# Kernel optimization log

Measured on AMD Instinct MI355X. Metric: run time of the kernel, lower is better.

The kernel has to match this reference:

```python
import jax, jax.numpy as jnp
import numpy as np

N, E, IN, H, C, ED = 50000, 400000, 128, 16, 32, 16
NEG_SLOPE = 0.2

def setup_inputs() -> dict:
    key = jax.random.key(0)
    ks = jax.random.split(key, 9)
    x = jax.random.normal(ks[0], (N, IN), jnp.float32)
    edge_index = jax.random.randint(ks[1], (2, E), 0, N, dtype=jnp.int32)
    edge_attr = jax.random.normal(ks[2], (E, ED), jnp.float32)
    batch = jnp.zeros((N,), jnp.int32)
    W_l = jax.random.normal(ks[3], (IN, H * C), jnp.float32) * 0.05
    W_r = jax.random.normal(ks[4], (IN, H * C), jnp.float32) * 0.05
    att = jax.random.normal(ks[5], (H, C), jnp.float32) * 0.05
    bias_gat = jax.random.normal(ks[6], (C,), jnp.float32) * 0.05
    W_res = jax.random.normal(ks[7], (IN, C), jnp.float32) * 0.05
    return {"x": x, "edge_index": edge_index, "edge_attr": edge_attr, "batch": batch,
            "W_l": W_l, "W_r": W_r, "att": att, "bias_gat": bias_gat, "W_res": W_res}

def reference(x, edge_index, edge_attr, batch, W_l, W_r, att, bias_gat, W_res):
    # GATv2Conv (heads=16, concat=False, add_self_loops=True, edge_dim=None so
    # edge_attr is unused; dropout is inference no-op), then ReLU + projected residual.
    n = x.shape[0]
    loops = jnp.arange(n, dtype=edge_index.dtype)
    src = jnp.concatenate([edge_index[0], loops])  # message source j
    dst = jnp.concatenate([edge_index[1], loops])  # message target i
    xl = (x @ W_l).reshape(n, H, C)  # source transform
    xr = (x @ W_r).reshape(n, H, C)  # target transform
    # GATv2 score: e_ij = a^T LeakyReLU(xl_j + xr_i), per head. [Etot, H]
    e = jnp.einsum('ehc,hc->eh', jax.nn.leaky_relu(xl[src] + xr[dst], NEG_SLOPE), att)
    # segment softmax over incoming edges of each destination node
    m = jax.lax.stop_gradient(jax.ops.segment_max(e, dst, num_segments=n))
    ex = jnp.exp(e - m[dst])
    s = jax.ops.segment_sum(ex, dst, num_segments=n)
    alpha = ex / (s[dst] + 1e-16)  # [Etot, H]
    # weighted scatter-aggregate of source messages
    out = jax.ops.segment_sum(xl[src] * alpha[:, :, None], dst, num_segments=n)  # [N, H, C]
    gat_out = out.mean(axis=1) + bias_gat  # concat=False -> head mean, + bias
    x_out = jax.nn.relu(gat_out) + x @ W_res  # ReLU then SkipConnection projection
    return (x_out, alpha)
```

## Files before the change

### kernel.cpp

```cpp
#include <hip/hip_runtime.h>
#include <hip/hip_bf16.h>

typedef unsigned int u32;
typedef unsigned short u16;

typedef __attribute__((ext_vector_type(8))) short bf16x8;
typedef __attribute__((ext_vector_type(4))) float f32x4;
typedef __attribute__((ext_vector_type(2))) float f32x2;

__device__ __forceinline__ float bflo(u32 p){ union{u32 u; float f;} v; v.u = p << 16; return v.f; }
__device__ __forceinline__ float bfhi(u32 p){ union{u32 u; float f;} v; v.u = p & 0xFFFF0000u; return v.f; }
__device__ __forceinline__ u16 f2bf(float f){
    union{float f; u32 u;} v; v.f = f;
    u32 r = (v.u + 0x7FFFu + ((v.u >> 16) & 1u)) >> 16;
    return (u16)r;
}
__device__ __forceinline__ u32 pack2(float a, float b){
    return ((u32)f2bf(a)) | (((u32)f2bf(b)) << 16);
}

#define HH 16
#define CC 32
#define HC 512
#define KIN 128
#define CT 1056
#define RESCALE_THR 8.0f

__global__ __launch_bounds__(256) void k_prep(
    const float* __restrict__ x, const float* __restrict__ Wl,
    const float* __restrict__ Wr, const float* __restrict__ Wres,
    u16* __restrict__ xb, u16* __restrict__ wbt_frag, int* __restrict__ counts,
    int xq, int N)
{
    int t = blockIdx.x * 256 + threadIdx.x;
    if (t < xq) {
        const float4* src = (const float4*)(x + (size_t)t * 8);
        float4 a = src[0], b = src[1];
        uint4 o;
        o.x = pack2(a.x, a.y); o.y = pack2(a.z, a.w);
        o.z = pack2(b.x, b.y); o.w = pack2(b.z, b.w);
        ((uint4*)xb)[t] = o;
    } else if (t < xq + CT * 128) {
        int u = t - xq;
        int c = u >> 7;
        int k = u & 127;
        float v;
        if (c < 512)       v = Wl[(size_t)k * 512 + c];
        else if (c < 1024) v = Wr[(size_t)k * 512 + (c - 512)];
        else               v = Wres[(size_t)k * 32 + (c - 1024)];
        int e    = k & 7;
        int krow = k >> 3;
        int kk   = krow >> 2;
        int lane = ((krow & 3) << 4) | (c & 15);
        int ct   = c >> 4;
        wbt_frag[(((size_t)ct * 4 + kk) * 64 + lane) * 8 + e] = f2bf(v);
    } else if (t < xq + CT * 128 + N) {
        counts[t - xq - CT * 128] = 0;
    }
}

__global__ __launch_bounds__(256) void k_mfma(
    const u16* __restrict__ xb, const u16* __restrict__ wbt_frag,
    u16* __restrict__ xl, u16* __restrict__ xr, float* __restrict__ xres,
    int N, int nrb)
{
    __shared__ u16 sh[128 * 128];
    const int i = blockIdx.x;
    const int xcd = i & 7;
    const int j = i >> 3;
    const int rb = xcd + 8 * (j / 9);
    const int cb = j % 9;
    if (rb >= nrb) return;
    const int tid = threadIdx.x;
    const int wave = tid >> 6, lane = tid & 63;
    const int row0 = rb * 128;

    uint4 zero = {0, 0, 0, 0};
    #pragma unroll
    for (int it = 0; it < 8; it++) {
        int idx = tid + it * 256;
        int r = idx >> 4, ch = idx & 15;
        int grow = row0 + r;
        uint4 v = (grow < N) ? ((const uint4*)(xb + (size_t)grow * KIN))[ch] : zero;
        *(uint4*)(sh + r * 128 + ((ch ^ (r & 7)) * 8)) = v;
    }
    __syncthreads();

    bf16x8 afrag[2][4];
    #pragma unroll
    for (int mt = 0; mt < 2; mt++) {
        #pragma unroll
        for (int kk = 0; kk < 4; kk++) {
            int r = wave * 32 + mt * 16 + (lane & 15);
            int chunk = (kk * 4 + (lane >> 4)) ^ (r & 7);
            afrag[mt][kk] = *(const bf16x8*)(sh + r * 128 + chunk * 8);
        }
    }
    __syncthreads();

    if (cb < 8) {
        #pragma unroll
        for (int nt = 0; nt < 8; nt++) {
            int ct = cb * 8 + nt;
            const bf16x8* bp = (const bf16x8*)(wbt_frag + (((size_t)ct * 4) * 64 + lane) * 8);
            f32x4 acc0 = {0, 0, 0, 0}, acc1 = {0, 0, 0, 0};
            #pragma unroll
            for (int kk = 0; kk < 4; kk++) {
                bf16x8 bfrag = bp[kk * 64];
                acc0 = __builtin_amdgcn_mfma_f32_16x16x32_bf16(afrag[0][kk], bfrag, acc0, 0, 0, 0);
                acc1 = __builtin_amdgcn_mfma_f32_16x16x32_bf16(afrag[1][kk], bfrag, acc1, 0, 0, 0);
            }
            int lcol = nt * 16 + (lane & 15);
            int ch = lcol >> 3, cin = lcol & 7;
            #pragma unroll
            for (int mt = 0; mt < 2; mt++) {
                f32x4 a = (mt == 0) ? acc0 : acc1;
                int rbase = wave * 32 + mt * 16 + (lane >> 4) * 4;
                #pragma unroll
                for (int jj = 0; jj < 4; jj++) {
                    int row = rbase + jj;
                    int chs = ch ^ ((row >> 2) & 3);
                    sh[row * 128 + chs * 8 + cin] = f2bf(a[jj]);
                }
            }
        }
        __syncthreads();
        u16* out = (cb < 4) ? xl : xr;
        const int colbase = (cb & 3) * 128;
        #pragma unroll
        for (int it = 0; it < 8; it++) {
            int idx = tid + it * 256;
            int r = idx >> 4, ch = idx & 15;
            int grow = row0 + r;
            if (grow < N) {
                int chs = ch ^ ((r >> 2) & 3);
                uint4 v = *(const uint4*)(sh + r * 128 + chs * 8);
                *(uint4*)(out + (size_t)grow * HC + colbase + ch * 8) = v;
            }
        }
    } else {
        #pragma unroll
        for (int nt = 0; nt < 2; nt++) {
            int ct = 64 + nt;
            const bf16x8* bp = (const bf16x8*)(wbt_frag + (((size_t)ct * 4) * 64 + lane) * 8);
            f32x4 acc0 = {0, 0, 0, 0}, acc1 = {0, 0, 0, 0};
            #pragma unroll
            for (int kk = 0; kk < 4; kk++) {
                bf16x8 bfrag = bp[kk * 64];
                acc0 = __builtin_amdgcn_mfma_f32_16x16x32_bf16(afrag[0][kk], bfrag, acc0, 0, 0, 0);
                acc1 = __builtin_amdgcn_mfma_f32_16x16x32_bf16(afrag[1][kk], bfrag, acc1, 0, 0, 0);
            }
            int c_out = nt * 16 + (lane & 15);
            #pragma unroll
            for (int mt = 0; mt < 2; mt++) {
                f32x4 a = (mt == 0) ? acc0 : acc1;
                int rbse = row0 + wave * 32 + mt * 16 + (lane >> 4) * 4;
                #pragma unroll
                for (int jj = 0; jj < 4; jj++) {
                    int grow = rbse + jj;
                    if (grow < N) xres[(size_t)grow * CC + c_out] = a[jj];
                }
            }
        }
    }
}

__global__ __launch_bounds__(256) void k_count(
    const int* __restrict__ ei, int* __restrict__ counts, int E, int N)
{
    int e = blockIdx.x * 256 + threadIdx.x;
    if (e >= E + N) return;
    int dst = (e < E) ? ei[E + e] : e - E;
    atomicAdd(&counts[dst], 1);
}

__global__ __launch_bounds__(1024) void k_scan1(
    const int* __restrict__ counts, int* __restrict__ offs, int* __restrict__ partials, int N)
{
    __shared__ int sh[1024];
    int i = blockIdx.x * 1024 + threadIdx.x;
    int v = (i < N) ? counts[i] : 0;
    sh[threadIdx.x] = v;
    __syncthreads();
    for (int off = 1; off < 1024; off <<= 1) {
        int t = (threadIdx.x >= off) ? sh[threadIdx.x - off] : 0;
        __syncthreads();
        sh[threadIdx.x] += t;
        __syncthreads();
    }
    if (i < N) offs[i] = sh[threadIdx.x] - v;
    if (threadIdx.x == 1023) partials[blockIdx.x] = sh[1023];
}

__global__ __launch_bounds__(1024) void k_scan3f(
    int* __restrict__ offs, const int* __restrict__ partials,
    int* __restrict__ cursor, int N, int nb)
{
    __shared__ int sbase;
    if (threadIdx.x < 64) {
        int k = threadIdx.x;
        int v = (k < nb && k < blockIdx.x) ? partials[k] : 0;
        #pragma unroll
        for (int st = 1; st < 64; st <<= 1) v += __shfl_xor(v, st);
        if (threadIdx.x == 0) sbase = v;
    }
    __syncthreads();
    int i = blockIdx.x * 1024 + threadIdx.x;
    if (i < N) {
        int o = offs[i] + sbase;
        offs[i] = o;
        cursor[i] = o;
    }
}

__global__ __launch_bounds__(256) void k_scatter(
    const int* __restrict__ ei, int* __restrict__ cursor,
    int* __restrict__ src_sorted, int* __restrict__ eid_sorted, int E, int N)
{
    int e = blockIdx.x * 256 + threadIdx.x;
    if (e >= E + N) return;
    int src, dst;
    if (e < E) { src = ei[e]; dst = ei[E + e]; }
    else       { src = e - E; dst = src; }
    int pos = atomicAdd(&cursor[dst], 1);
    src_sorted[pos] = src;
    eid_sorted[pos] = e;
}

__global__ __launch_bounds__(64) void k_fused(
    const int* __restrict__ src_sorted, const int* __restrict__ eid_sorted,
    const int* __restrict__ offs, const int* __restrict__ counts,
    const u16* __restrict__ xl, const u16* __restrict__ xr, const float* __restrict__ att,
    float* __restrict__ e_out, float2* __restrict__ ms_buf,
    float* __restrict__ out_mean, int N)
{
    const int node = blockIdx.x;
    const int lane = threadIdx.x;
    const int h = lane >> 2;

    uint4 b = ((const uint4*)(xr + (size_t)node * HC))[lane];
    f32x2 xr0 = {bflo(b.x), bfhi(b.x)}, xr1 = {bflo(b.y), bfhi(b.y)};
    f32x2 xr2 = {bflo(b.z), bfhi(b.z)}, xr3 = {bflo(b.w), bfhi(b.w)};
    float4 w0 = ((const float4*)att)[lane * 2];
    float4 w1 = ((const float4*)att)[lane * 2 + 1];
    f32x2 wv0 = {w0.x, w0.y}, wv1 = {w0.z, w0.w};
    f32x2 wv2 = {w1.x, w1.y}, wv3 = {w1.z, w1.w};

    float m = -3.402823466e38f, s = 0.f;
    f32x2 ac0 = {0,0}, ac1 = {0,0}, ac2 = {0,0}, ac3 = {0,0};

    const int beg = offs[node];
    const int deg = counts[node];

    int sv = src_sorted[beg];
    uint4 a = ((const uint4*)(xl + (size_t)sv * HC))[lane];
    for (int t = 0; t < deg; t++) {
        uint4 acr = a;
        int sn = src_sorted[beg + min(t + 1, deg - 1)];
        a = ((const uint4*)(xl + (size_t)sn * HC))[lane];

        f32x2 xv0 = {bflo(acr.x), bfhi(acr.x)};
        f32x2 xv1 = {bflo(acr.y), bfhi(acr.y)};
        f32x2 xv2 = {bflo(acr.z), bfhi(acr.z)};
        f32x2 xv3 = {bflo(acr.w), bfhi(acr.w)};

        f32x2 es2 = {0.f, 0.f};
        f32x2 v;
        v = xv0 + xr0; v = __builtin_elementwise_max(v, 0.2f * v); es2 = __builtin_elementwise_fma(v, wv0, es2);
        v = xv1 + xr1; v = __builtin_elementwise_max(v, 0.2f * v); es2 = __builtin_elementwise_fma(v, wv1, es2);
        v = xv2 + xr2; v = __builtin_elementwise_max(v, 0.2f * v); es2 = __builtin_elementwise_fma(v, wv2, es2);
        v = xv3 + xr3; v = __builtin_elementwise_max(v, 0.2f * v); es2 = __builtin_elementwise_fma(v, wv3, es2);
        float esum = es2.x + es2.y;
        esum += __shfl_xor(esum, 1);
        esum += __shfl_xor(esum, 2);

        int eid = eid_sorted[beg + t];
        if ((lane & 3) == 0)
            e_out[(size_t)eid * HH + h] = esum;

        if (__any(esum > m + RESCALE_THR)) {
            float mn = fmaxf(m, esum);
            float sc = __expf(m - mn);
            float p  = __expf(esum - mn);
            s = s * sc + p;
            m = mn;
            f32x2 p2 = {p, p}, sc2 = {sc, sc};
            ac0 = __builtin_elementwise_fma(p2, xv0, ac0 * sc2);
            ac1 = __builtin_elementwise_fma(p2, xv1, ac1 * sc2);
            ac2 = __builtin_elementwise_fma(p2, xv2, ac2 * sc2);
            ac3 = __builtin_elementwise_fma(p2, xv3, ac3 * sc2);
        } else {
            float p = __expf(esum - m);
            s += p;
            f32x2 p2 = {p, p};
            ac0 = __builtin_elementwise_fma(p2, xv0, ac0);
            ac1 = __builtin_elementwise_fma(p2, xv1, ac1);
            ac2 = __builtin_elementwise_fma(p2, xv2, ac2);
            ac3 = __builtin_elementwise_fma(p2, xv3, ac3);
        }
    }

    float inv = 1.f / (s + 1e-16f);
    if ((lane & 3) == 0)
        ms_buf[(size_t)node * HH + h] = make_float2(m, inv);

    float acc[8] = { ac0.x * inv, ac0.y * inv, ac1.x * inv, ac1.y * inv,
                     ac2.x * inv, ac2.y * inv, ac3.x * inv, ac3.y * inv };
    #pragma unroll
    for (int st = 4; st <= 32; st <<= 1) {
        #pragma unroll
        for (int q = 0; q < 8; q++) acc[q] += __shfl_xor(acc[q], st);
    }
    if (lane < 4) {
        float* dp = out_mean + (size_t)node * CC + lane * 8;
        #pragma unroll
        for (int q = 0; q < 8; q++) dp[q] = acc[q];
    }
}

__global__ __launch_bounds__(256) void k_alphafinal(
    const int* __restrict__ ei, float* __restrict__ alpha,
    const float2* __restrict__ ms_buf, const float* __restrict__ out_mean,
    const float* __restrict__ xres, const float* __restrict__ bias,
    float* __restrict__ x_out, int E, int N)
{
    long long i = (long long)blockIdx.x * 256 + threadIdx.x;
    if (i < (long long)N * CC) {
        int c = (int)(i & 31);
        float g = out_mean[i] * (1.f / 16.f) + bias[c];
        g = g > 0.f ? g : 0.f;
        x_out[i] = g + xres[i];
    }
    long long tot = (long long)(E + N) * HH;
    if (i < tot) {
        int edge = (int)(i >> 4);
        int h = (int)(i & 15);
        int dst = (edge < E) ? ei[E + edge] : edge - E;
        float2 ms = ms_buf[(size_t)dst * HH + h];
        alpha[i] = __expf(alpha[i] - ms.x) * ms.y;
    }
}

extern "C" void kernel_launch(void* const* d_in, const int* in_sizes, int n_in,
                              void* d_out, int out_size, void* d_ws, size_t ws_size,
                              hipStream_t stream)
{
    const int N = in_sizes[0] / KIN;
    const int E = in_sizes[1] / 2;
    const int Etot = E + N;

    const float* x    = (const float*)d_in[0];
    const int*   ei   = (const int*)d_in[1];
    const float* Wl   = (const float*)d_in[4];
    const float* Wr   = (const float*)d_in[5];
    const float* att  = (const float*)d_in[6];
    const float* bias = (const float*)d_in[7];
    const float* Wres = (const float*)d_in[8];

    char* ws = (char*)d_ws;
    u16*   xl         = (u16*)ws;   ws += (size_t)N * HC * 2;
    u16*   xr         = (u16*)ws;   ws += (size_t)N * HC * 2;
    float2* ms_buf    = (float2*)ws; ws += (size_t)N * HH * 8;
    float* xres       = (float*)ws; ws += (size_t)N * CC * 4;
    float* out_mean   = (float*)ws; ws += (size_t)N * CC * 4;
    int*   counts     = (int*)ws;   ws += (size_t)N * 4;
    int*   offs       = (int*)ws;   ws += (size_t)N * 4;
    int*   cursor     = (int*)ws;   ws += (size_t)N * 4;
    int*   partials   = (int*)ws;   ws += 256;
    int*   src_sorted = (int*)ws;   ws += (size_t)Etot * 4;
    int*   eid_sorted = (int*)ws;   ws += (size_t)Etot * 4;
    u16*   xb         = (u16*)ws;   ws += (size_t)N * KIN * 2;
    u16*   wbt_frag   = (u16*)ws;   ws += (size_t)CT * KIN * 2;

    float* x_out     = (float*)d_out;
    float* alpha_out = x_out + (size_t)N * CC;

    int xq = N * KIN / 8;
    int ptot = xq + CT * 128 + N;
    k_prep<<<(ptot + 255) / 256, 256, 0, stream>>>(
        x, Wl, Wr, Wres, xb, wbt_frag, counts, xq, N);

    int nrb = (N + 127) / 128;
    int mgrid = 8 * ((nrb + 7) / 8) * 9;
    k_mfma<<<mgrid, 256, 0, stream>>>(xb, wbt_frag, xl, xr, xres, N, nrb);

    int eg = (Etot + 255) / 256;
    k_count<<<eg, 256, 0, stream>>>(ei, counts, E, N);
    int nb = (N + 1023) / 1024;
    k_scan1<<<nb, 1024, 0, stream>>>(counts, offs, partials, N);
    k_scan3f<<<nb, 1024, 0, stream>>>(offs, partials, cursor, N, nb);
    k_scatter<<<eg, 256, 0, stream>>>(ei, cursor, src_sorted, eid_sorted, E, N);

    k_fused<<<N, 64, 0, stream>>>(
        src_sorted, eid_sorted, offs, counts, xl, xr, att,
        alpha_out, ms_buf, out_mean, N);

    long long tot = (long long)Etot * HH;
    k_alphafinal<<<(int)((tot + 255) / 256), 256, 0, stream>>>(
        ei, alpha_out, ms_buf, out_mean, xres, bias, x_out, E, N);
}
```

Baseline: 190.0 us.

## Interleave xl/xr column layout to write MFMA results directly, fold residual block

The GEMM kernel now writes MFMA accumulator outputs straight to global memory as packed bf16 pairs from two adjacent column tiles, dropping the LDS staging pass and its barriers. This permutes the column layout of xl/xr, and the fused attention kernel's att loading and out_mean store are adjusted to match. The residual projection block is merged into the last column block, giving 8 blocks per row band instead of 9. Direct 4-byte strided global stores may coalesce worse than the previous 16-byte staged writes, and the cb==7 blocks now carry extra work.

```diff
diff --git a/kernel.cpp b/kernel.cpp
--- a/kernel.cpp
+++ b/kernel.cpp
@@ -25,6 +25,7 @@
 #define KIN 128
 #define CT 1056
 #define RESCALE_THR 8.0f
+
 
 __global__ __launch_bounds__(256) void k_prep(
     const float* __restrict__ x, const float* __restrict__ Wl,
@@ -68,8 +69,8 @@
     const int i = blockIdx.x;
     const int xcd = i & 7;
     const int j = i >> 3;
-    const int rb = xcd + 8 * (j / 9);
-    const int cb = j % 9;
+    const int rb = xcd + 8 * (j >> 3);
+    const int cb = j & 7;
     if (rb >= nrb) return;
     const int tid = threadIdx.x;
     const int wave = tid >> 6, lane = tid & 63;
@@ -96,54 +97,46 @@
             afrag[mt][kk] = *(const bf16x8*)(sh + r * 128 + chunk * 8);
         }
     }
-    __syncthreads();
-
-    if (cb < 8) {
-        #pragma unroll
-        for (int nt = 0; nt < 8; nt++) {
-            int ct = cb * 8 + nt;
-            const bf16x8* bp = (const bf16x8*)(wbt_frag + (((size_t)ct * 4) * 64 + lane) * 8);
-            f32x4 acc0 = {0, 0, 0, 0}, acc1 = {0, 0, 0, 0};
+
+    u32* out = (u32*)((cb < 4) ? xl : xr);
+    const int cbu = (cb & 3) * 64;
+
+    #pragma unroll
+    for (int ntp = 0; ntp < 4; ntp++) {
+        int ctA = cb * 8 + 2 * ntp;
+        const bf16x8* bpA = (const bf16x8*)(wbt_frag + (((size_t)ctA * 4) * 64 + lane) * 8);
+        const bf16x8* bpB = (const bf16x8*)(wbt_frag + (((size_t)(ctA + 1) * 4) * 64 + lane) * 8);
+        f32x4 aA0 = {0,0,0,0}, aA1 = {0,0,0,0}, aB0 = {0,0,0,0}, aB1 = {0,0,0,0};
+        #pragma unroll
+        for (int kk = 0; kk < 4; kk++) {
+            bf16x8 bA = bpA[kk * 64];
+            bf16x8 bB = bpB[kk * 64];
+            aA0 = __builtin_amdgcn_mfma_f32_16x16x32_bf16(afrag[0][kk], bA, aA0, 0, 0, 0);
+            aA1 = __builtin_amdgcn_mfma_f32_16x16x32_bf16(afrag[1][kk], bA, aA1, 0, 0, 0);
+            aB0 = __builtin_amdgcn_mfma_f32_16x16x32_bf16(afrag[0][kk], bB, aB0, 0, 0, 0);
+            aB1 = __builtin_amdgcn_mfma_f32_16x16x32_bf16(afrag[1][kk], bB, aB1, 0, 0, 0);
+        }
+        int ucol = cbu + ntp * 16 + (lane & 15);
+        #pragma unroll
+        for (int mt = 0; mt < 2; mt++) {
+            f32x4 vA = (mt == 0) ? aA0 : aA1;
+            f32x4 vB = (mt == 0) ? aB0 : aB1;
+            int rbase = row0 + wave * 32 + mt * 16 + (lane >> 4) * 4;
             #pragma unroll
-            for (int kk = 0; kk < 4; kk++) {
-                bf16x8 bfrag = bp[kk * 64];
-                acc0 = __builtin_amdgcn_mfma_f32_16x16x32_bf16(afrag[0][kk], bfrag, acc0, 0, 0, 0);
-                acc1 = __builtin_amdgcn_mfma_f32_16x16x32_bf16(afrag[1][kk], bfrag, acc1, 0, 0, 0);
+            for (int jj = 0; jj < 4; jj++) {
+                int grow = rbase + jj;
+                if (grow < N)
+                    out[(size_t)grow * 256 + ucol] = pack2(vA[jj], vB[jj]);
             }
-            int lcol = nt * 16 + (lane & 15);
-            int ch = lcol >> 3, cin = lcol & 7;
-            #pragma unroll
-            for (int mt = 0; mt < 2; mt++) {
-                f32x4 a = (mt == 0) ? acc0 : acc1;
-                int rbase = wave * 32 + mt * 16 + (lane >> 4) * 4;
-                #pragma unroll
-                for (int jj = 0; jj < 4; jj++) {
-                    int row = rbase + jj;
-                    int chs = ch ^ ((row >> 2) & 3);
-                    sh[row * 128 + chs * 8 + cin] = f2bf(a[jj]);
-                }
-            }
-        }
-        __syncthreads();
-        u16* out = (cb < 4) ? xl : xr;
-        const int colbase = (cb & 3) * 128;
-        #pragma unroll
-        for (int it = 0; it < 8; it++) {
-            int idx = tid + it * 256;
-            int r = idx >> 4, ch = idx & 15;
-            int grow = row0 + r;
-            if (grow < N) {
-                int chs = ch ^ ((r >> 2) & 3);
-                uint4 v = *(const uint4*)(sh + r * 128 + chs * 8);
-                *(uint4*)(out + (size_t)grow * HC + colbase + ch * 8) = v;
-            }
-        }
-    } else {
+        }
+    }
+
+    if (cb == 7) {
         #pragma unroll
         for (int nt = 0; nt < 2; nt++) {
             int ct = 64 + nt;
             const bf16x8* bp = (const bf16x8*)(wbt_frag + (((size_t)ct * 4) * 64 + lane) * 8);
-            f32x4 acc0 = {0, 0, 0, 0}, acc1 = {0, 0, 0, 0};
+            f32x4 acc0 = {0,0,0,0}, acc1 = {0,0,0,0};
             #pragma unroll
             for (int kk = 0; kk < 4; kk++) {
                 bf16x8 bfrag = bp[kk * 64];
@@ -237,14 +230,16 @@
     const int node = blockIdx.x;
     const int lane = threadIdx.x;
     const int h = lane >> 2;
+    const int q = lane & 3;
 
     uint4 b = ((const uint4*)(xr + (size_t)node * HC))[lane];
     f32x2 xr0 = {bflo(b.x), bfhi(b.x)}, xr1 = {bflo(b.y), bfhi(b.y)};
     f32x2 xr2 = {bflo(b.z), bfhi(b.z)}, xr3 = {bflo(b.w), bfhi(b.w)};
-    float4 w0 = ((const float4*)att)[lane * 2];
-    float4 w1 = ((const float4*)att)[lane * 2 + 1];
-    f32x2 wv0 = {w0.x, w0.y}, wv1 = {w0.z, w0.w};
-    f32x2 wv2 = {w1.x, w1.y}, wv3 = {w1.z, w1.w};
+    const float4* att4 = (const float4*)att;
+    float4 wlo = att4[8 * h + q];
+    float4 whi = att4[8 * h + 4 + q];
+    f32x2 wv0 = {wlo.x, whi.x}, wv1 = {wlo.y, whi.y};
+    f32x2 wv2 = {wlo.z, whi.z}, wv3 = {wlo.w, whi.w};
 
     float m = -3.402823466e38f, s = 0.f;
     f32x2 ac0 = {0,0}, ac1 = {0,0}, ac2 = {0,0}, ac3 = {0,0};
@@ -275,7 +270,7 @@
         esum += __shfl_xor(esum, 2);
 
         int eid = eid_sorted[beg + t];
-        if ((lane & 3) == 0)
+        if (q == 0)
             e_out[(size_t)eid * HH + h] = esum;
 
         if (__any(esum > m + RESCALE_THR)) {
@@ -301,7 +296,7 @@
     }
 
     float inv = 1.f / (s + 1e-16f);
-    if ((lane & 3) == 0)
+    if (q == 0)
         ms_buf[(size_t)node * HH + h] = make_float2(m, inv);
 
     float acc[8] = { ac0.x * inv, ac0.y * inv, ac1.x * inv, ac1.y * inv,
@@ -309,12 +304,14 @@
     #pragma unroll
     for (int st = 4; st <= 32; st <<= 1) {
         #pragma unroll
-        for (int q = 0; q < 8; q++) acc[q] += __shfl_xor(acc[q], st);
+        for (int qq = 0; qq < 8; qq++) acc[qq] += __shfl_xor(acc[qq], st);
     }
     if (lane < 4) {
-        float* dp = out_mean + (size_t)node * CC + lane * 8;
-        #pragma unroll
-        for (int q = 0; q < 8; q++) dp[q] = acc[q];
+        float4* dp4 = (float4*)(out_mean + (size_t)node * CC);
+        float4 lo = { acc[0], acc[2], acc[4], acc[6] };
+        float4 hi = { acc[1], acc[3], acc[5], acc[7] };
+        dp4[lane] = lo;
+        dp4[4 + lane] = hi;
     }
 }
 
@@ -381,7 +378,7 @@
         x, Wl, Wr, Wres, xb, wbt_frag, counts, xq, N);
 
     int nrb = (N + 127) / 128;
-    int mgrid = 8 * ((nrb + 7) / 8) * 9;
+    int mgrid = 8 * ((nrb + 7) / 8) * 8;
     k_mfma<<<mgrid, 256, 0, stream>>>(xb, wbt_frag, xl, xr, xres, N, nrb);
 
     int eg = (Etot + 255) / 256;
```

Result: slower. 197.8 us (+4.1%).
